# Performance work log

Measured on AMD Instinct MI355X. Metric: run time of the kernel, lower is better.

## Reference

```python
import jax, jax.numpy as jnp
import numpy as np

B, S, D, O = 8, 2048, 1024, 1024  # batch, seq_len, state_dim(=input_dim), output_dim


def setup_inputs() -> dict:
    key = jax.random.key(0)
    k_in, k_a, k_bc = jax.random.split(key, 3)
    inputs = jax.random.normal(k_in, (B, S, D), dtype=jnp.float32)
    # Stable diagonal transition (|A| < 1) so the 2048-step recurrence stays bounded.
    A = jax.random.uniform(k_a, (D,), minval=-0.99, maxval=0.99, dtype=jnp.float32)
    BC = jax.random.normal(k_bc, (D, O), dtype=jnp.float32) / D
    return {"inputs": inputs, "A": A, "BC": BC}


def reference(inputs, A, BC):
    # Diagonal LTI recurrence: h_t = A * h_{t-1} + x_t ; out_t = h_t @ BC
    # h0 = zeros (the module's h0 Parameter is initialized to zeros).
    x_tfirst = jnp.swapaxes(inputs, 0, 1)  # [S, B, D]

    def step(h, x_t):
        h = h * A + x_t
        return h, h

    h0 = jnp.zeros((inputs.shape[0], A.shape[0]), dtype=inputs.dtype)
    _, hs = jax.lax.scan(step, h0, x_tfirst)  # hs: [S, B, D]
    # Single fused projection over all timesteps instead of per-step matmuls.
    out = jnp.einsum('sbd,do->bso', hs, BC)  # [B, S, O]
    return out
```

## Files before the change

### kernel.cpp

```cpp
#include <hip/hip_runtime.h>
#include <hip/hip_bf16.h>

#define BB 8
#define SS 2048
#define DD 1024
#define OO 1024
#define MM (BB * SS)
#define KK DD
#define NN OO
#define CC 64
#define LL 32

typedef __bf16 bf16x8 __attribute__((ext_vector_type(8)));
typedef __bf16 bf16x4 __attribute__((ext_vector_type(4)));
typedef float floatx4 __attribute__((ext_vector_type(4)));

__device__ __forceinline__ float4 fma4(float4 h, float4 a, float4 v) {
    h.x = fmaf(h.x, a.x, v.x);
    h.y = fmaf(h.y, a.y, v.y);
    h.z = fmaf(h.z, a.z, v.z);
    h.w = fmaf(h.w, a.w, v.w);
    return h;
}

__global__ __launch_bounds__(256) void prep(const float* __restrict__ x,
                                            const float* __restrict__ A,
                                            float* __restrict__ carry,
                                            const float* __restrict__ BC,
                                            __bf16* __restrict__ BCt) {
    __shared__ float tile[32][33];
    const int id = blockIdx.x;
    if (id < BB * CC) {
        const int c = id & (CC - 1);
        const int b = id >> 6;
        const int i4 = threadIdx.x;
        const float4 a = ((const float4*)A)[i4];
        const float4* xp = (const float4*)(x + ((size_t)b * SS + (size_t)c * LL) * DD) + i4;
        float4 h = make_float4(0.f, 0.f, 0.f, 0.f);
#pragma unroll
        for (int t0 = 0; t0 < LL; t0 += 8) {
            float4 v[8];
#pragma unroll
            for (int u = 0; u < 8; ++u) v[u] = xp[(size_t)(t0 + u) * (DD / 4)];
#pragma unroll
            for (int u = 0; u < 8; ++u) h = fma4(h, a, v[u]);
        }
        ((float4*)carry)[((size_t)b * CC + c) * (DD / 4) + i4] = h;
    } else {
        const int t = id - BB * CC;
        const int o0 = (t & 31) * 32;
        const int d0 = (t >> 5) * 32;
        const int tx = threadIdx.x & 31;
        const int ty = threadIdx.x >> 5;
#pragma unroll
        for (int i = 0; i < 4; ++i) {
            const int dd = ty + i * 8;
            tile[dd][tx] = BC[(size_t)(d0 + dd) * OO + o0 + tx];
        }
        __syncthreads();
#pragma unroll
        for (int i = 0; i < 4; ++i) {
            const int oo = ty + i * 8;
            BCt[(size_t)(o0 + oo) * DD + d0 + tx] = (__bf16)tile[tx][oo];
        }
    }
}

__global__ __launch_bounds__(256) void scan_emit(const float* __restrict__ x,
                                                 const float* __restrict__ A,
                                                 const float* __restrict__ carry,
                                                 __bf16* __restrict__ hs) {
    const int id = blockIdx.x;
    const int c = id & (CC - 1);
    const int b = id >> 6;
    const int i4 = threadIdx.x;
    const float4 a = ((const float4*)A)[i4];
    float4 aL = a;
#pragma unroll
    for (int i = 0; i < 5; ++i) { aL.x *= aL.x; aL.y *= aL.y; aL.z *= aL.z; aL.w *= aL.w; }
    float4 h = make_float4(0.f, 0.f, 0.f, 0.f);
    const float4* cp = (const float4*)carry + (size_t)b * CC * (DD / 4) + i4;
    for (int j = 0; j < c; ++j) {
        const float4 cv = cp[(size_t)j * (DD / 4)];
        h.x = fmaf(h.x, aL.x, cv.x);
        h.y = fmaf(h.y, aL.y, cv.y);
        h.z = fmaf(h.z, aL.z, cv.z);
        h.w = fmaf(h.w, aL.w, cv.w);
    }
    const size_t base = ((size_t)b * SS + (size_t)c * LL) * DD;
    const float4* xp = (const float4*)(x + base) + i4;
    bf16x4* hp = (bf16x4*)(hs + base) + i4;
#pragma unroll
    for (int t0 = 0; t0 < LL; t0 += 8) {
        float4 v[8];
#pragma unroll
        for (int u = 0; u < 8; ++u) v[u] = xp[(size_t)(t0 + u) * (DD / 4)];
#pragma unroll
        for (int u = 0; u < 8; ++u) {
            h = fma4(h, a, v[u]);
            bf16x4 o;
            o[0] = (__bf16)h.x; o[1] = (__bf16)h.y; o[2] = (__bf16)h.z; o[3] = (__bf16)h.w;
            hp[(size_t)(t0 + u) * (DD / 4)] = o;
        }
    }
}

#define TM 128
#define TN 128
#define TK 32
#define NITER (KK / TK)

__device__ __forceinline__ void async16(void* lds, const void* g) {
    __builtin_amdgcn_global_load_lds(
        (__attribute__((address_space(1))) void*)(void*)g,
        (__attribute__((address_space(3))) void*)lds, 16, 0, 0);
}

__global__ __launch_bounds__(256) void gemm_bt(const __bf16* __restrict__ Am,
                                               const __bf16* __restrict__ Bt,
                                               float* __restrict__ C) {
    __shared__ __align__(16) __bf16 As[2][TM * TK];
    __shared__ __align__(16) __bf16 Bs[2][TN * TK];

    const int tid = threadIdx.x;
    const int wave = tid >> 6;
    const int lane = tid & 63;
    const int wm = (wave >> 1) * 64;
    const int wn = (wave & 1) * 64;
    const int lanelo = lane & 15;
    const int quad = lane >> 4;
    const int tile_m = blockIdx.x * TM;
    const int tile_n = blockIdx.y * TN;

    const int cid0 = tid;
    const int cid1 = tid + 256;
    const int r0 = cid0 >> 2, q0 = ((cid0 & 3) ^ ((r0 >> 1) & 3)) * 8;
    const int r1 = cid1 >> 2, q1 = ((cid1 & 3) ^ ((r1 >> 1) & 3)) * 8;

    const __bf16* Ab  = Am + (size_t)(tile_m + r0) * KK + q0;
    const __bf16* Ab1 = Am + (size_t)(tile_m + r1) * KK + q1;
    const __bf16* Bb  = Bt + (size_t)(tile_n + r0) * KK + q0;
    const __bf16* Bb1 = Bt + (size_t)(tile_n + r1) * KK + q1;

    const int fs = (lanelo >> 1) & 3;
    const int kq = (quad ^ fs) * 8;

    floatx4 acc[4][4];
#pragma unroll
    for (int i = 0; i < 4; ++i)
#pragma unroll
        for (int j = 0; j < 4; ++j) acc[i][j] = (floatx4){0.f, 0.f, 0.f, 0.f};

    async16(&As[0][cid0 * 8], Ab);
    async16(&As[0][cid1 * 8], Ab1);
    async16(&Bs[0][cid0 * 8], Bb);
    async16(&Bs[0][cid1 * 8], Bb1);

    int cur = 0;
    for (int i = 0; i < NITER; ++i) {
        __syncthreads();
        if (i + 1 < NITER) {
            const int k = (i + 1) * TK;
            async16(&As[cur ^ 1][cid0 * 8], Ab + k);
            async16(&As[cur ^ 1][cid1 * 8], Ab1 + k);
            async16(&Bs[cur ^ 1][cid0 * 8], Bb + k);
            async16(&Bs[cur ^ 1][cid1 * 8], Bb1 + k);
        }

        bf16x8 af[4], bf[4];
#pragma unroll
        for (int ii = 0; ii < 4; ++ii)
            af[ii] = *(const bf16x8*)(&As[cur][(wm + ii * 16 + lanelo) * TK + kq]);
#pragma unroll
        for (int j = 0; j < 4; ++j)
            bf[j] = *(const bf16x8*)(&Bs[cur][(wn + j * 16 + lanelo) * TK + kq]);

#pragma unroll
        for (int ii = 0; ii < 4; ++ii)
#pragma unroll
            for (int j = 0; j < 4; ++j)
                acc[ii][j] = __builtin_amdgcn_mfma_f32_16x16x32_bf16(af[ii], bf[j], acc[ii][j], 0, 0, 0);
        cur ^= 1;
    }

#pragma unroll
    for (int i = 0; i < 4; ++i) {
        const int row = tile_m + wm + i * 16 + quad * 4;
#pragma unroll
        for (int r = 0; r < 4; ++r) {
            float* crow = C + (size_t)(row + r) * NN + tile_n + wn + lanelo;
#pragma unroll
            for (int j = 0; j < 4; ++j) crow[j * 16] = acc[i][j][r];
        }
    }
}

extern "C" void kernel_launch(void* const* d_in, const int* in_sizes, int n_in,
                              void* d_out, int out_size, void* d_ws, size_t ws_size,
                              hipStream_t stream) {
    const float* x  = (const float*)d_in[0];
    const float* A  = (const float*)d_in[1];
    const float* BC = (const float*)d_in[2];
    float* out = (float*)d_out;

    char* ws = (char*)d_ws;
    __bf16* hs   = (__bf16*)ws;
    float* carry = (float*)(ws + 33554432);
    __bf16* BCt  = (__bf16*)(ws + 33554432 + 2097152);

    prep<<<dim3(BB * CC + 1024), 256, 0, stream>>>(x, A, carry, BC, BCt);
    scan_emit<<<dim3(BB * CC), 256, 0, stream>>>(x, A, carry, hs);
    gemm_bt<<<dim3(MM / TM, NN / TN), 256, 0, stream>>>(hs, BCt, out);
}
```

Before: 178.1 us.

## Enlarge GEMM tiles to 256x256x64 with XCD-aware mapping and vmcnt-pipelined prefetch

```diff
diff --git a/kernel.cpp b/kernel.cpp
--- a/kernel.cpp
+++ b/kernel.cpp
@@ -105,10 +105,10 @@
     }
 }
 
-#define TM 128
-#define TN 128
-#define TK 32
-#define NITER (KK / TK)
+#define GTM 256
+#define GTN 256
+#define GTK 64
+#define GNT (KK / GTK)
 
 __device__ __forceinline__ void async16(void* lds, const void* g) {
     __builtin_amdgcn_global_load_lds(
@@ -116,75 +116,97 @@
         (__attribute__((address_space(3))) void*)lds, 16, 0, 0);
 }
 
-__global__ __launch_bounds__(256) void gemm_bt(const __bf16* __restrict__ Am,
-                                               const __bf16* __restrict__ Bt,
-                                               float* __restrict__ C) {
-    __shared__ __align__(16) __bf16 As[2][TM * TK];
-    __shared__ __align__(16) __bf16 Bs[2][TN * TK];
+#define MEMFENCE asm volatile("" ::: "memory")
+#define BARRIER do { MEMFENCE; __builtin_amdgcn_s_barrier(); MEMFENCE; } while (0)
+
+__global__ __launch_bounds__(512, 2) void gemm_bt(const __bf16* __restrict__ Am,
+                                                  const __bf16* __restrict__ Bt,
+                                                  float* __restrict__ C) {
+    __shared__ __align__(16) __bf16 As[2][GTM * GTK];
+    __shared__ __align__(16) __bf16 Bs[2][GTN * GTK];
 
     const int tid = threadIdx.x;
     const int wave = tid >> 6;
     const int lane = tid & 63;
-    const int wm = (wave >> 1) * 64;
-    const int wn = (wave & 1) * 64;
+    const int wm = (wave >> 2) * 128;
+    const int wn = (wave & 3) * 64;
     const int lanelo = lane & 15;
     const int quad = lane >> 4;
-    const int tile_m = blockIdx.x * TM;
-    const int tile_n = blockIdx.y * TN;
-
-    const int cid0 = tid;
-    const int cid1 = tid + 256;
-    const int r0 = cid0 >> 2, q0 = ((cid0 & 3) ^ ((r0 >> 1) & 3)) * 8;
-    const int r1 = cid1 >> 2, q1 = ((cid1 & 3) ^ ((r1 >> 1) & 3)) * 8;
-
-    const __bf16* Ab  = Am + (size_t)(tile_m + r0) * KK + q0;
-    const __bf16* Ab1 = Am + (size_t)(tile_m + r1) * KK + q1;
-    const __bf16* Bb  = Bt + (size_t)(tile_n + r0) * KK + q0;
-    const __bf16* Bb1 = Bt + (size_t)(tile_n + r1) * KK + q1;
-
-    const int fs = (lanelo >> 1) & 3;
-    const int kq = (quad ^ fs) * 8;
-
-    floatx4 acc[4][4];
-#pragma unroll
-    for (int i = 0; i < 4; ++i)
+
+    const int bid = blockIdx.x;
+    const int xcd = bid & 7;
+    const int loc = bid >> 3;
+    const int tile_m = (xcd * 8 + (loc >> 2)) * GTM;
+    const int tile_n = (loc & 3) * GTN;
+
+    const __bf16* Abp[4];
+    const __bf16* Bbp[4];
+#pragma unroll
+    for (int j = 0; j < 4; ++j) {
+        const int cid = tid + j * 512;
+        const int r = cid >> 3;
+        const int qg = ((cid & 7) ^ (r & 7)) * 8;
+        Abp[j] = Am + (size_t)(tile_m + r) * KK + qg;
+        Bbp[j] = Bt + (size_t)(tile_n + r) * KK + qg;
+    }
+
+    floatx4 acc[8][4];
+#pragma unroll
+    for (int i = 0; i < 8; ++i)
 #pragma unroll
         for (int j = 0; j < 4; ++j) acc[i][j] = (floatx4){0.f, 0.f, 0.f, 0.f};
 
-    async16(&As[0][cid0 * 8], Ab);
-    async16(&As[0][cid1 * 8], Ab1);
-    async16(&Bs[0][cid0 * 8], Bb);
-    async16(&Bs[0][cid1 * 8], Bb1);
-
-    int cur = 0;
-    for (int i = 0; i < NITER; ++i) {
-        __syncthreads();
-        if (i + 1 < NITER) {
-            const int k = (i + 1) * TK;
-            async16(&As[cur ^ 1][cid0 * 8], Ab + k);
-            async16(&As[cur ^ 1][cid1 * 8], Ab1 + k);
-            async16(&Bs[cur ^ 1][cid0 * 8], Bb + k);
-            async16(&Bs[cur ^ 1][cid1 * 8], Bb1 + k);
-        }
-
-        bf16x8 af[4], bf[4];
-#pragma unroll
-        for (int ii = 0; ii < 4; ++ii)
-            af[ii] = *(const bf16x8*)(&As[cur][(wm + ii * 16 + lanelo) * TK + kq]);
+    auto stage = [&](int t, int u) {
+        const int k = t * GTK;
 #pragma unroll
         for (int j = 0; j < 4; ++j)
-            bf[j] = *(const bf16x8*)(&Bs[cur][(wn + j * 16 + lanelo) * TK + kq]);
-
-#pragma unroll
-        for (int ii = 0; ii < 4; ++ii)
-#pragma unroll
-            for (int j = 0; j < 4; ++j)
-                acc[ii][j] = __builtin_amdgcn_mfma_f32_16x16x32_bf16(af[ii], bf[j], acc[ii][j], 0, 0, 0);
-        cur ^= 1;
-    }
-
-#pragma unroll
-    for (int i = 0; i < 4; ++i) {
+            async16(&As[u][(tid + j * 512) * 8], Abp[j] + k);
+#pragma unroll
+        for (int j = 0; j < 4; ++j)
+            async16(&Bs[u][(tid + j * 512) * 8], Bbp[j] + k);
+    };
+
+    auto compute = [&](int u) {
+        const __bf16* as = As[u];
+        const __bf16* bs = Bs[u];
+#pragma unroll
+        for (int kk = 0; kk < 2; ++kk) {
+            bf16x8 af[8], bv[4];
+#pragma unroll
+            for (int ii = 0; ii < 8; ++ii) {
+                const int row = wm + ii * 16 + lanelo;
+                af[ii] = *(const bf16x8*)(as + row * GTK + ((((kk << 2) | quad) ^ (lanelo & 7)) * 8));
+            }
+#pragma unroll
+            for (int j = 0; j < 4; ++j) {
+                const int row = wn + j * 16 + lanelo;
+                bv[j] = *(const bf16x8*)(bs + row * GTK + ((((kk << 2) | quad) ^ (lanelo & 7)) * 8));
+            }
+            __builtin_amdgcn_s_setprio(1);
+#pragma unroll
+            for (int ii = 0; ii < 8; ++ii)
+#pragma unroll
+                for (int j = 0; j < 4; ++j)
+                    acc[ii][j] = __builtin_amdgcn_mfma_f32_16x16x32_bf16(af[ii], bv[j], acc[ii][j], 0, 0, 0);
+            __builtin_amdgcn_s_setprio(0);
+        }
+    };
+
+    stage(0, 0);
+
+    for (int t = 0; t < GNT - 1; ++t) {
+        stage(t + 1, (t + 1) & 1);
+        asm volatile("s_waitcnt vmcnt(8)" ::: "memory");
+        BARRIER;
+        compute(t & 1);
+        BARRIER;
+    }
+    asm volatile("s_waitcnt vmcnt(0)" ::: "memory");
+    BARRIER;
+    compute((GNT - 1) & 1);
+
+#pragma unroll
+    for (int i = 0; i < 8; ++i) {
         const int row = tile_m + wm + i * 16 + quad * 4;
 #pragma unroll
         for (int r = 0; r < 4; ++r) {
@@ -210,5 +232,5 @@
 
     prep<<<dim3(BB * CC + 1024), 256, 0, stream>>>(x, A, carry, BC, BCt);
     scan_emit<<<dim3(BB * CC), 256, 0, stream>>>(x, A, carry, hs);
-    gemm_bt<<<dim3(MM / TM, NN / TN), 256, 0, stream>>>(hs, BCt, out);
-}
+    gemm_bt<<<dim3(256), 512, 0, stream>>>(hs, BCt, out);
+}
```

Result: faster. 167.5 us (-5.9%).
